# Performance work log

Measured on AMD Instinct MI355X. Metric: run time of the kernel, lower is better.

The kernel has to match this reference:

```python
import jax, jax.numpy as jnp
import numpy as np

N = 4096   # num_nodes == nb_items
E = 3      # num_edge types
C = 2      # num_channels
D = 128    # basket_embed_dim
RU = 128   # rnn_units
B = 32     # batch size
L = 20     # max_seq_length
ALPHA = 0.5


def _gtconv(W, A):
    # softmax over edge types, then channel-weighted combine of adjacencies
    f = jax.nn.softmax(W, axis=1)              # [C, E]
    return jnp.einsum('ce,enm->cnm', f, A)     # [C, N, N]


def _normalize(H):
    # remove self loops, then column-degree (in-degree) inverse normalization
    eye = jnp.eye(H.shape[-1], dtype=H.dtype)
    Hn = H * (1.0 - eye)
    deg = Hn.sum(axis=1)                        # scatter_add over col -> [C, N]
    dinv = jnp.where(deg == 0, jnp.zeros_like(deg), 1.0 / deg)
    dinv = jax.lax.stop_gradient(dinv)          # original computes deg under no_grad
    return Hn * dinv[:, None, :]


def _lstm(x, h0, c0, W_ih, W_hh, b_ih, b_hh):
    # single-layer batch-first LSTM, torch gate order (i, f, g, o)
    def step(carry, xt):
        h, c = carry
        z = xt @ W_ih.T + b_ih + h @ W_hh.T + b_hh
        i, f, g, o = jnp.split(z, 4, axis=-1)
        c = jax.nn.sigmoid(f) * c + jax.nn.sigmoid(i) * jnp.tanh(g)
        h = jax.nn.sigmoid(o) * jnp.tanh(c)
        return (h, c), h
    _, ys = jax.lax.scan(step, (h0, c0), jnp.swapaxes(x, 0, 1))
    return jnp.swapaxes(ys, 0, 1)               # [B, L, RU]


def setup_inputs():
    key = jax.random.key(0)
    k = jax.random.split(key, 12)
    A = jax.random.uniform(k[0], (E, N, N), jnp.float32) * (2.0 / N)
    seqs = (jax.random.uniform(k[1], (B, L, N)) < 0.02).astype(jnp.float32)
    seq_len = jax.random.randint(k[2], (B,), 1, L + 1)
    h0 = jnp.zeros((B, RU), jnp.float32)
    c0 = jnp.zeros((B, RU), jnp.float32)
    W1a = 1.0 + 0.1 * jax.random.normal(k[3], (C, E), jnp.float32)
    W1b = 1.0 + 0.1 * jax.random.normal(k[4], (C, E), jnp.float32)
    W2 = 1.0 + 0.1 * jax.random.normal(k[5], (C, E), jnp.float32)
    I_B = jnp.ones((N,), jnp.float32) / N
    lin_w = jax.random.normal(k[6], (C, D, N), jnp.float32) / np.sqrt(N).astype(np.float32)
    lin_b = jnp.zeros((C, D), jnp.float32)
    proj_w = jax.random.normal(k[7], (D, C * D), jnp.float32) / np.sqrt(C * D).astype(np.float32)
    proj_b = jnp.zeros((D,), jnp.float32)
    W_ih = jax.random.normal(k[8], (4 * RU, D), jnp.float32) / np.sqrt(D).astype(np.float32)
    W_hh = jax.random.normal(k[9], (4 * RU, RU), jnp.float32) / np.sqrt(RU).astype(np.float32)
    b_ih = jnp.zeros((4 * RU,), jnp.float32)
    b_hh = jnp.zeros((4 * RU,), jnp.float32)
    h2item_w = jax.random.normal(k[10], (N, RU), jnp.float32) / np.sqrt(RU).astype(np.float32)
    return dict(A=A, seqs=seqs, seq_len=seq_len, h0=h0, c0=c0, W1a=W1a, W1b=W1b,
                W2=W2, I_B=I_B, lin_w=lin_w, lin_b=lin_b, proj_w=proj_w, proj_b=proj_b,
                W_ih=W_ih, W_hh=W_hh, b_ih=b_ih, b_hh=b_hh, h2item_w=h2item_w)


def reference(A, seqs, seq_len, h0, c0, W1a, W1b, W2, I_B, lin_w, lin_b,
              proj_w, proj_b, W_ih, W_hh, b_ih, b_hh, h2item_w):
    # layer 0 (first=True): H[c] = conv1(A)[c] @ conv2(A)[c]  (spspmm, dense form)
    H = jnp.einsum('cij,cjk->cik', _gtconv(W1a, A), _gtconv(W1b, A))
    # layer 1: H[c] = norm(H)[c] @ conv(A)[c]
    H = jnp.einsum('cij,cjk->cik', _normalize(H), _gtconv(W2, A))

    x = seqs.reshape(-1, N)                     # [B*L, nb_items]
    v = jax.nn.relu(I_B)                        # diag(I_B) after relu
    enc = []
    for i in range(C):
        xh = jax.nn.relu(x @ H[i])
        if i == 0:
            e = jax.nn.relu(x * v) + xh         # note: channel-0 formula differs
        else:
            e = jax.nn.relu(x * v + xh)
        enc.append(e @ lin_w[i].T + lin_b[i])
    enc = jnp.concatenate(enc, axis=1)          # [B*L, C*D]
    baskets = (enc @ proj_w.T + proj_b).reshape(B, L, D)

    lstm_out = _lstm(baskets, h0, c0, W_ih, W_hh, b_ih, b_hh)
    idx = jnp.arange(B) * L + (seq_len - 1)
    last = lstm_out.reshape(-1, RU)[idx]        # [B, RU]
    probs = jax.nn.sigmoid(last @ h2item_w.T)   # [B, nb_items]
    return (1.0 - ALPHA) * probs + ALPHA * (probs * v)
```

## Files before the change

### kernel.cpp

```cpp
#include <hip/hip_runtime.h>


typedef float  f4v  __attribute__((ext_vector_type(4)));
typedef short  s8v  __attribute__((ext_vector_type(8)));
typedef unsigned short u16;
typedef u16    us4  __attribute__((ext_vector_type(4)));

#define NN 4096
#define MM 640

__device__ __forceinline__ u16 f2bf(float f){
  unsigned int u = __float_as_uint(f);
  u += 0x7FFFu + ((u>>16)&1u);
  return (u16)(u>>16);
}
__device__ __forceinline__ float bf2f(u16 h){ return __uint_as_float(((unsigned int)h)<<16); }
__device__ __forceinline__ float sigm(float x){ return 1.f/(1.f+__expf(-x)); }

__device__ __forceinline__ void gload16(const void* g, void* l){
  __builtin_amdgcn_global_load_lds((const __attribute__((address_space(1))) unsigned int*)g,
                                   (__attribute__((address_space(3))) unsigned int*)l, 16, 0, 0);
}

__device__ __forceinline__ void softmax23(const float* __restrict__ W, float f[2][3]){
  #pragma unroll
  for (int c=0;c<2;c++){
    float a=W[c*3+0], b=W[c*3+1], d=W[c*3+2];
    float m=fmaxf(a,fmaxf(b,d));
    float ea=__expf(a-m), eb=__expf(b-m), ed=__expf(d-m);
    float s=1.f/(ea+eb+ed);
    f[c][0]=ea*s; f[c][1]=eb*s; f[c][2]=ed*s;
  }
}

template<int PH3>
__global__ __launch_bounds__(256)
void k_combine(const float* __restrict__ A, const float* __restrict__ Wa,
               const float* __restrict__ Wb, u16* __restrict__ C1,
               u16* __restrict__ Ct, float* __restrict__ r)
{
  __shared__ u16 t2[2][64][68];
  __shared__ float rs[2][64];
  const int tid = threadIdx.x;
  const int n0 = blockIdx.x*64, m0 = blockIdx.y*64;
  float fa[2][3], fb[2][3];
  softmax23(Wa, fa);
  if constexpr(!PH3) softmax23(Wb, fb);
  if constexpr(!PH3){ if (tid < 128) rs[tid>>6][tid&63] = 0.f; }
  __syncthreads();
  const int cl = (tid&15)*4, rw0 = tid>>4;
  float rp[2][4] = {};
  #pragma unroll
  for (int q=0;q<4;q++){
    const int m = q*16 + rw0;
    const float* ap = A + (size_t)(m0+m)*NN + n0 + cl;
    f4v a0 = *(const f4v*)ap;
    f4v a1 = *(const f4v*)(ap + (size_t)NN*NN);
    f4v a2 = *(const f4v*)(ap + 2*(size_t)NN*NN);
    #pragma unroll
    for (int c=0;c<2;c++){
      f4v vt;
      if constexpr(!PH3){
        f4v v1 = fa[c][0]*a0 + fa[c][1]*a1 + fa[c][2]*a2;
        vt     = fb[c][0]*a0 + fb[c][1]*a1 + fb[c][2]*a2;
        us4 o;
        #pragma unroll
        for (int k=0;k<4;k++){ o[k]=f2bf(v1[k]); rp[c][k]+=v1[k]; }
        *(us4*)(C1 + ((size_t)c*NN + m0+m)*NN + n0+cl) = o;
      } else {
        vt = fa[c][0]*a0 + fa[c][1]*a1 + fa[c][2]*a2;
      }
      #pragma unroll
      for (int k=0;k<4;k++) t2[c][cl+k][m] = f2bf(vt[k]);
    }
  }
  if constexpr(!PH3){
    #pragma unroll
    for (int c=0;c<2;c++)
      #pragma unroll
      for (int k=0;k<4;k++) atomicAdd(&rs[c][cl+k], rp[c][k]);
  }
  __syncthreads();
  if constexpr(!PH3){
    if (tid < 128) atomicAdd(&r[(size_t)(tid>>6)*NN + n0 + (tid&63)], rs[tid>>6][tid&63]);
  }
  #pragma unroll
  for (int q=0;q<4;q++){
    const int nl = q*16 + rw0;
    #pragma unroll
    for (int c=0;c<2;c++){
      us4 o = *(const us4*)&t2[c][nl][cl];
      *(us4*)(Ct + ((size_t)c*NN + n0+nl)*NN + m0+cl) = o;
    }
  }
}

__global__ __launch_bounds__(256)
void k_sparse_y(const float* __restrict__ seqs, const u16* __restrict__ C1,
                u16* __restrict__ y)
{
  __shared__ int idxl[512];
  __shared__ int cnt;
  const int tid = threadIdx.x, row = blockIdx.x;
  if (tid==0) cnt = 0;
  __syncthreads();
  const float* xr = seqs + (size_t)row*NN;
  #pragma unroll
  for (int it=0; it<4; ++it){
    f4v v = *(const f4v*)(xr + it*1024 + tid*4);
    #pragma unroll
    for (int k=0;k<4;k++) if (v[k] > 0.5f){ int p = atomicAdd(&cnt,1); if (p<512) idxl[p] = it*1024+tid*4+k; }
  }
  __syncthreads();
  const int nz = cnt < 512 ? cnt : 512;
  float acc0[16], acc1[16];
  #pragma unroll
  for (int k=0;k<16;k++){ acc0[k]=0.f; acc1[k]=0.f; }
  const int cb = tid*16;
  for (int p=0;p<nz;++p){
    const u16* r0 = C1 + (size_t)idxl[p]*NN + cb;
    const u16* r1 = r0 + (size_t)NN*NN;
    s8v a = *(const s8v*)r0, b = *(const s8v*)(r0+8);
    s8v c = *(const s8v*)r1, d = *(const s8v*)(r1+8);
    #pragma unroll
    for (int k=0;k<8;k++){
      acc0[k]   += bf2f((u16)a[k]);
      acc0[8+k] += bf2f((u16)b[k]);
      acc1[k]   += bf2f((u16)c[k]);
      acc1[8+k] += bf2f((u16)d[k]);
    }
  }
  s8v o0,o1,o2,o3;
  #pragma unroll
  for (int k=0;k<8;k++){
    o0[k]=(short)f2bf(acc0[k]);   o1[k]=(short)f2bf(acc0[8+k]);
    o2[k]=(short)f2bf(acc1[k]);   o3[k]=(short)f2bf(acc1[8+k]);
  }
  u16* y0 = y + (size_t)row*NN + cb;
  *(s8v*)y0 = o0; *(s8v*)(y0+8) = o1;
  u16* y1 = y0 + (size_t)MM*NN;
  *(s8v*)y1 = o2; *(s8v*)(y1+8) = o3;
}

__global__ __launch_bounds__(256)
void k_diagdeg(const u16* __restrict__ C1, const u16* __restrict__ C2t,
               const float* __restrict__ r, float* __restrict__ diag1,
               float* __restrict__ dinv)
{
  const int tid = threadIdx.x, lane = tid&63;
  const int gw = blockIdx.x*4 + (tid>>6);
  const int c = gw>>12, k = gw&4095;
  const u16* p1 = C1  + ((size_t)c*NN + k)*NN;
  const u16* p2 = C2t + ((size_t)c*NN + k)*NN;
  const float* pr = r + (size_t)c*NN;
  float dd = 0.f, dg = 0.f;
  for (int it=0; it<8; ++it){
    const int j = it*512 + lane*8;
    s8v v1 = *(const s8v*)(p1+j);
    s8v v2 = *(const s8v*)(p2+j);
    f4v r0 = *(const f4v*)(pr+j);
    f4v r1 = *(const f4v*)(pr+j+4);
    #pragma unroll
    for (int q=0;q<8;q++){
      float c2 = bf2f((u16)v2[q]);
      dd += bf2f((u16)v1[q]) * c2;
      dg += ((q<4)? r0[q] : r1[q-4]) * c2;
    }
  }
  #pragma unroll
  for (int m=1;m<64;m<<=1){ dd += __shfl_xor(dd, m); dg += __shfl_xor(dg, m); }
  if (lane==0){
    float deg = dg - dd;
    diag1[(size_t)c*NN+k] = dd;
    dinv[(size_t)c*NN+k]  = (deg==0.f) ? 0.f : 1.f/deg;
  }
}

template<int EPI>
__global__ __launch_bounds__(256)
void k_gemm(const u16* __restrict__ Xb, const u16* __restrict__ Bt,
            const float* __restrict__ seqs, const float* __restrict__ diag1,
            const float* __restrict__ dinv, const float* __restrict__ IB,
            u16* __restrict__ outp)
{
  __shared__ u16 As[128*32];
  __shared__ u16 Bs[128*32];
  const int tid = threadIdx.x, lane = tid&63, w = tid>>6;
  const int c = blockIdx.z, m0 = blockIdx.x*128, n0 = blockIdx.y*128;
  const u16* Ab = Xb + (size_t)c*MM*NN;
  const u16* Bb = Bt + (size_t)c*NN*NN;
  const int srow = lane>>2, skof = (lane&3)*8;
  const int fr = lane&15, fk = (lane>>4)*8;
  const int wm = (w>>1)*64, wn = (w&1)*64;
  f4v acc[4][4];
  #pragma unroll
  for (int i=0;i<4;i++)
    #pragma unroll
    for (int j=0;j<4;j++) acc[i][j] = (f4v){0.f,0.f,0.f,0.f};
  for (int k0=0;k0<NN;k0+=32){
    gload16(Ab + (size_t)(m0 +      w*16 + srow)*NN + k0 + skof, (void*)&As[(     w*16)*32]);
    gload16(Ab + (size_t)(m0 + 64 + w*16 + srow)*NN + k0 + skof, (void*)&As[(64 + w*16)*32]);
    gload16(Bb + (size_t)(n0 +      w*16 + srow)*NN + k0 + skof, (void*)&Bs[(     w*16)*32]);
    gload16(Bb + (size_t)(n0 + 64 + w*16 + srow)*NN + k0 + skof, (void*)&Bs[(64 + w*16)*32]);
    __syncthreads();
    s8v a[4], b[4];
    #pragma unroll
    for (int t=0;t<4;t++) a[t] = *(const s8v*)&As[(wm + t*16 + fr)*32 + fk];
    #pragma unroll
    for (int t=0;t<4;t++) b[t] = *(const s8v*)&Bs[(wn + t*16 + fr)*32 + fk];
    #pragma unroll
    for (int i=0;i<4;i++)
      #pragma unroll
      for (int j=0;j<4;j++)
        acc[i][j] = __builtin_amdgcn_mfma_f32_16x16x32_bf16(a[i], b[j], acc[i][j], 0, 0, 0);
    __syncthreads();
  }
  #pragma unroll
  for (int i=0;i<4;i++){
    #pragma unroll
    for (int j=0;j<4;j++){
      const int col = n0 + wn + j*16 + fr;
      #pragma unroll
      for (int rr=0;rr<4;rr++){
        const int row = m0 + wm + i*16 + (lane>>4)*4 + rr;
        const float z = acc[i][j][rr];
        const float x = seqs[(size_t)row*NN + col];
        float val;
        if constexpr(EPI==0){
          val = (z - x*diag1[(size_t)c*NN+col]) * dinv[(size_t)c*NN+col];
        } else {
          float xh = fmaxf(z, 0.f);
          float vv = fmaxf(IB[col], 0.f);
          val = (c==0) ? (fmaxf(x*vv,0.f) + xh) : fmaxf(x*vv + xh, 0.f);
        }
        outp[((size_t)c*MM + row)*NN + col] = f2bf(val);
      }
    }
  }
}

__global__ __launch_bounds__(256)
void k_cvt(const float* __restrict__ linw, const float* __restrict__ whh,
           u16* __restrict__ linwb, u16* __restrict__ whhb)
{
  const int g = blockIdx.x*256 + threadIdx.x;
  const int i = g*4;
  const int NL = 2*128*NN;
  f4v v; u16* dst;
  if (i < NL){ v = *(const f4v*)(linw + i); dst = linwb + i; }
  else       { v = *(const f4v*)(whh + (i-NL)); dst = whhb + (i-NL); }
  us4 o;
  #pragma unroll
  for (int k=0;k<4;k++) o[k]=f2bf(v[k]);
  *(us4*)dst = o;
}

__global__ __launch_bounds__(256)
void k_lin(const u16* __restrict__ e, const u16* __restrict__ linwb,
           float* __restrict__ encr)
{
  __shared__ u16 As[64*32];
  __shared__ u16 Bs[64*32];
  const int tid=threadIdx.x, lane=tid&63, w=tid>>6;
  const int m0 = blockIdx.x*64, d0 = blockIdx.y*64;
  const int c = blockIdx.z>>2, ks = blockIdx.z&3;
  const u16* Ab = e + (size_t)c*MM*NN;
  const u16* Bb = linwb + (size_t)c*128*NN;
  const int srow=lane>>2, skof=(lane&3)*8, fr=lane&15, fk=(lane>>4)*8;
  const int wm=(w>>1)*32, wn=(w&1)*32;
  f4v acc[2][2];
  #pragma unroll
  for (int i=0;i<2;i++)
    #pragma unroll
    for (int j=0;j<2;j++) acc[i][j] = (f4v){0.f,0.f,0.f,0.f};
  for (int ki=0;ki<32;++ki){
    const int k0 = ks*1024 + ki*32;
    gload16(Ab + (size_t)(m0 + w*16 + srow)*NN + k0 + skof, (void*)&As[(w*16)*32]);
    gload16(Bb + (size_t)(d0 + w*16 + srow)*NN + k0 + skof, (void*)&Bs[(w*16)*32]);
    __syncthreads();
    s8v a[2], b[2];
    #pragma unroll
    for (int t=0;t<2;t++) a[t] = *(const s8v*)&As[(wm+t*16+fr)*32+fk];
    #pragma unroll
    for (int t=0;t<2;t++) b[t] = *(const s8v*)&Bs[(wn+t*16+fr)*32+fk];
    #pragma unroll
    for (int i=0;i<2;i++)
      #pragma unroll
      for (int j=0;j<2;j++)
        acc[i][j] = __builtin_amdgcn_mfma_f32_16x16x32_bf16(a[i], b[j], acc[i][j], 0, 0, 0);
    __syncthreads();
  }
  #pragma unroll
  for (int i=0;i<2;i++)
    #pragma unroll
    for (int j=0;j<2;j++){
      const int col = d0 + wn + j*16 + fr;
      #pragma unroll
      for (int rr=0;rr<4;rr++){
        const int row = m0 + wm + i*16 + (lane>>4)*4 + rr;
        atomicAdd(&encr[(size_t)row*256 + c*128 + col], acc[i][j][rr]);
      }
    }
}

__global__ __launch_bounds__(256)
void k_proj(const float* __restrict__ encr, const float* __restrict__ linb,
            const float* __restrict__ pw, const float* __restrict__ pb,
            float* __restrict__ bask)
{
  const int g = blockIdx.x*256 + threadIdx.x;
  const int row = g>>7, d = g&127;
  const float* er = encr + (size_t)row*256;
  const float* wr = pw + (size_t)d*256;
  float acc = pb[d];
  for (int j=0;j<256;j+=4){
    f4v e4 = *(const f4v*)(er+j);
    f4v l4 = *(const f4v*)(linb+j);
    f4v w4 = *(const f4v*)(wr+j);
    acc += (e4[0]+l4[0])*w4[0] + (e4[1]+l4[1])*w4[1] + (e4[2]+l4[2])*w4[2] + (e4[3]+l4[3])*w4[3];
  }
  bask[g] = acc;
}

__global__ __launch_bounds__(256)
void k_xhat(const float* __restrict__ bask, const float* __restrict__ wih,
            const float* __restrict__ bih, const float* __restrict__ bhh,
            float* __restrict__ xh)
{
  const int g = blockIdx.x*256 + threadIdx.x;
  const int row = g>>9, n = g&511;
  const float* br = bask + (size_t)row*128;
  const float* wr = wih + (size_t)n*128;
  float acc = bih[n] + bhh[n];
  for (int k=0;k<128;k+=4){
    f4v b4=*(const f4v*)(br+k); f4v w4=*(const f4v*)(wr+k);
    acc += b4[0]*w4[0]+b4[1]*w4[1]+b4[2]*w4[2]+b4[3]*w4[3];
  }
  const int b = row/20, t = row%20;
  xh[((size_t)t*32 + b)*512 + n] = acc;
}

__global__ __launch_bounds__(512)
void k_lstm(const float* __restrict__ xhat, const u16* __restrict__ whhb,
            const float* __restrict__ h0, const float* __restrict__ c0,
            const int* __restrict__ slen, float* __restrict__ last)
{
  __shared__ float zb[32][512];
  __shared__ float cbuf[32][128];
  __shared__ u16 hb[32][136];
  const int tid = threadIdx.x, lane = tid&63, w = tid>>6;
  for (int i=tid; i<4096; i+=512){ int b=i>>7,u=i&127; cbuf[b][u]=c0[i]; hb[b][u]=f2bf(h0[i]); }
  const int fr = lane&15, fko = (lane>>4)*8;
  s8v bfr[4][4];
  #pragma unroll
  for (int nt=0;nt<4;nt++)
    #pragma unroll
    for (int kf=0;kf<4;kf++)
      bfr[nt][kf] = *(const s8v*)(whhb + (size_t)(w*64 + nt*16 + fr)*128 + kf*32 + fko);
  __syncthreads();
  for (int t=0;t<20;++t){
    s8v af[2][4];
    #pragma unroll
    for (int mt=0;mt<2;mt++)
      #pragma unroll
      for (int kf=0;kf<4;kf++)
        af[mt][kf] = *(const s8v*)&hb[mt*16+fr][kf*32+fko];
    f4v z[2][4];
    #pragma unroll
    for (int mt=0;mt<2;mt++)
      #pragma unroll
      for (int nt=0;nt<4;nt++){
        const int nn2 = w*64 + nt*16 + fr;
        #pragma unroll
        for (int rr=0;rr<4;rr++){
          const int bb = mt*16 + (lane>>4)*4 + rr;
          z[mt][nt][rr] = xhat[((size_t)t*32 + bb)*512 + nn2];
        }
      }
    #pragma unroll
    for (int kf=0;kf<4;kf++)
      #pragma unroll
      for (int mt=0;mt<2;mt++)
        #pragma unroll
        for (int nt=0;nt<4;nt++)
          z[mt][nt] = __builtin_amdgcn_mfma_f32_16x16x32_bf16(af[mt][kf], bfr[nt][kf], z[mt][nt], 0, 0, 0);
    #pragma unroll
    for (int mt=0;mt<2;mt++)
      #pragma unroll
      for (int nt=0;nt<4;nt++){
        const int nn2 = w*64 + nt*16 + fr;
        #pragma unroll
        for (int rr=0;rr<4;rr++){
          const int bb = mt*16 + (lane>>4)*4 + rr;
          zb[bb][nn2] = z[mt][nt][rr];
        }
      }
    __syncthreads();
    for (int p=tid; p<4096; p+=512){
      const int b=p>>7, u=p&127;
      float zi=zb[b][u], zf=zb[b][128+u], zg=zb[b][256+u], zo=zb[b][384+u];
      float ii=sigm(zi), ff=sigm(zf), gg=tanhf(zg), oo=sigm(zo);
      float cn = ff*cbuf[b][u] + ii*gg;
      float hn = oo*tanhf(cn);
      cbuf[b][u]=cn; hb[b][u]=f2bf(hn);
      if (t == slen[b]-1) last[p] = hn;
    }
    __syncthreads();
  }
}

__global__ __launch_bounds__(256)
void k_final(const float* __restrict__ last, const float* __restrict__ h2w,
             const float* __restrict__ IB, float* __restrict__ out)
{
  __shared__ float ls[128];
  const int b = blockIdx.y;
  const int n = blockIdx.x*256 + threadIdx.x;
  if (threadIdx.x < 128) ls[threadIdx.x] = last[b*128 + threadIdx.x];
  __syncthreads();
  const float* wr = h2w + (size_t)n*128;
  float acc = 0.f;
  for (int k=0;k<128;k+=4){
    f4v w4 = *(const f4v*)(wr+k);
    acc += w4[0]*ls[k] + w4[1]*ls[k+1] + w4[2]*ls[k+2] + w4[3]*ls[k+3];
  }
  const float vn = fmaxf(IB[n], 0.f);
  out[(size_t)b*NN + n] = (0.5f + 0.5f*vn) * sigm(acc);
}

extern "C" void kernel_launch(void* const* d_in, const int* in_sizes, int n_in,
                              void* d_out, int out_size, void* d_ws, size_t ws_size,
                              hipStream_t stream)
{
  const float* A    = (const float*)d_in[0];
  const float* seqs = (const float*)d_in[1];
  const int*   slen = (const int*)  d_in[2];
  const float* h0   = (const float*)d_in[3];
  const float* c0   = (const float*)d_in[4];
  const float* W1a  = (const float*)d_in[5];
  const float* W1b  = (const float*)d_in[6];
  const float* W2   = (const float*)d_in[7];
  const float* IB   = (const float*)d_in[8];
  const float* linw = (const float*)d_in[9];
  const float* linb = (const float*)d_in[10];
  const float* pw   = (const float*)d_in[11];
  const float* pb   = (const float*)d_in[12];
  const float* wih  = (const float*)d_in[13];
  const float* whh  = (const float*)d_in[14];
  const float* bih  = (const float*)d_in[15];
  const float* bhh  = (const float*)d_in[16];
  const float* h2w  = (const float*)d_in[17];
  (void)in_sizes; (void)n_in; (void)out_size; (void)ws_size;

  char* ws = (char*)d_ws;
  size_t off = 0;
  auto alloc = [&](size_t sz)->void*{ void* p = ws + off; off += (sz + 255) & ~(size_t)255; return p; };
  u16*   C1    = (u16*)  alloc((size_t)2*NN*NN*2);
  u16*   C2t   = (u16*)  alloc((size_t)2*NN*NN*2);
  u16*   y     = (u16*)  alloc((size_t)2*MM*NN*2);
  u16*   u     = (u16*)  alloc((size_t)2*MM*NN*2);
  float* r     = (float*)alloc((size_t)2*NN*4);
  float* diag1 = (float*)alloc((size_t)2*NN*4);
  float* dinv  = (float*)alloc((size_t)2*NN*4);
  u16*   linwb = (u16*)  alloc((size_t)2*128*NN*2);
  u16*   whhb  = (u16*)  alloc((size_t)512*128*2);
  float* encr  = (float*)alloc((size_t)MM*256*4);
  float* bask  = (float*)alloc((size_t)MM*128*4);
  float* xh    = (float*)alloc((size_t)20*32*512*4);
  float* last  = (float*)alloc((size_t)32*128*4);

  hipMemsetAsync(r, 0, (size_t)2*NN*4, stream);
  hipMemsetAsync(encr, 0, (size_t)MM*256*4, stream);

  k_combine<0><<<dim3(64,64),256,0,stream>>>(A, W1a, W1b, C1, C2t, r);
  k_sparse_y<<<MM,256,0,stream>>>(seqs, C1, y);
  k_diagdeg<<<2048,256,0,stream>>>(C1, C2t, r, diag1, dinv);
  k_gemm<0><<<dim3(5,32,2),256,0,stream>>>(y, C2t, seqs, diag1, dinv, IB, u);
  k_combine<1><<<dim3(64,64),256,0,stream>>>(A, W2, W2, C1, C1, r);
  u16* e = y;
  k_gemm<1><<<dim3(5,32,2),256,0,stream>>>(u, C1, seqs, diag1, dinv, IB, e);
  k_cvt<<<1088,256,0,stream>>>(linw, whh, linwb, whhb);
  k_lin<<<dim3(10,2,8),256,0,stream>>>(e, linwb, encr);
  k_proj<<<320,256,0,stream>>>(encr, linb, pw, pb, bask);
  k_xhat<<<1280,256,0,stream>>>(bask, wih, bih, bhh, xh);
  k_lstm<<<1,512,0,stream>>>(xh, whhb, h0, c0, slen, last);
  k_final<<<dim3(16,32),256,0,stream>>>(last, h2w, IB, (float*)d_out);
}
```

Before: 629.8 us.

## Split-K the dense GEMMs, swizzle LDS tiles, and fuse combine passes over A

Both dense 640x4096x4096 GEMMs now split K four ways, so the grid grows from 320 to 1280 blocks. Each block writes fp32 partial sums, and a separate epilogue kernel adds them and applies the normalization or relu logic. The K-tile doubles to 64 and uses an XOR-swizzled LDS layout to cut bank conflicts. The two passes over A that built the combined adjacencies are merged into one kernel that also produces the W2-combined transposed matrix, so A is read once. The cost is about 84 MB of fp32 partial traffic per GEMM, an extra 64 MB workspace matrix, and two more launches.

```diff
diff --git a/kernel.cpp b/kernel.cpp
--- a/kernel.cpp
+++ b/kernel.cpp
@@ -8,6 +8,8 @@
 
 #define NN 4096
 #define MM 640
+#define KSPL 4
+#define KCH (NN/KSPL)
 
 __device__ __forceinline__ u16 f2bf(float f){
   unsigned int u = __float_as_uint(f);
@@ -33,20 +35,22 @@
   }
 }
 
-template<int PH3>
-__global__ __launch_bounds__(256)
-void k_combine(const float* __restrict__ A, const float* __restrict__ Wa,
-               const float* __restrict__ Wb, u16* __restrict__ C1,
-               u16* __restrict__ Ct, float* __restrict__ r)
+__global__ __launch_bounds__(256)
+void k_combine_all(const float* __restrict__ A, const float* __restrict__ W1a,
+                   const float* __restrict__ W1b, const float* __restrict__ W2,
+                   u16* __restrict__ C1, u16* __restrict__ C2t,
+                   u16* __restrict__ C3t, float* __restrict__ r)
 {
   __shared__ u16 t2[2][64][68];
+  __shared__ u16 t3[2][64][68];
   __shared__ float rs[2][64];
   const int tid = threadIdx.x;
   const int n0 = blockIdx.x*64, m0 = blockIdx.y*64;
-  float fa[2][3], fb[2][3];
-  softmax23(Wa, fa);
-  if constexpr(!PH3) softmax23(Wb, fb);
-  if constexpr(!PH3){ if (tid < 128) rs[tid>>6][tid&63] = 0.f; }
+  float fa[2][3], fb[2][3], fc[2][3];
+  softmax23(W1a, fa);
+  softmax23(W1b, fb);
+  softmax23(W2,  fc);
+  if (tid < 128) rs[tid>>6][tid&63] = 0.f;
   __syncthreads();
   const int cl = (tid&15)*4, rw0 = tid>>4;
   float rp[2][4] = {};
@@ -59,38 +63,32 @@
     f4v a2 = *(const f4v*)(ap + 2*(size_t)NN*NN);
     #pragma unroll
     for (int c=0;c<2;c++){
-      f4v vt;
-      if constexpr(!PH3){
-        f4v v1 = fa[c][0]*a0 + fa[c][1]*a1 + fa[c][2]*a2;
-        vt     = fb[c][0]*a0 + fb[c][1]*a1 + fb[c][2]*a2;
-        us4 o;
-        #pragma unroll
-        for (int k=0;k<4;k++){ o[k]=f2bf(v1[k]); rp[c][k]+=v1[k]; }
-        *(us4*)(C1 + ((size_t)c*NN + m0+m)*NN + n0+cl) = o;
-      } else {
-        vt = fa[c][0]*a0 + fa[c][1]*a1 + fa[c][2]*a2;
-      }
-      #pragma unroll
-      for (int k=0;k<4;k++) t2[c][cl+k][m] = f2bf(vt[k]);
-    }
-  }
-  if constexpr(!PH3){
-    #pragma unroll
-    for (int c=0;c<2;c++)
-      #pragma unroll
-      for (int k=0;k<4;k++) atomicAdd(&rs[c][cl+k], rp[c][k]);
-  }
+      f4v v1 = fa[c][0]*a0 + fa[c][1]*a1 + fa[c][2]*a2;
+      f4v vt = fb[c][0]*a0 + fb[c][1]*a1 + fb[c][2]*a2;
+      f4v v3 = fc[c][0]*a0 + fc[c][1]*a1 + fc[c][2]*a2;
+      us4 o;
+      #pragma unroll
+      for (int k=0;k<4;k++){ o[k]=f2bf(v1[k]); rp[c][k]+=v1[k]; }
+      *(us4*)(C1 + ((size_t)c*NN + m0+m)*NN + n0+cl) = o;
+      #pragma unroll
+      for (int k=0;k<4;k++){ t2[c][cl+k][m] = f2bf(vt[k]); t3[c][cl+k][m] = f2bf(v3[k]); }
+    }
+  }
+  #pragma unroll
+  for (int c=0;c<2;c++)
+    #pragma unroll
+    for (int k=0;k<4;k++) atomicAdd(&rs[c][cl+k], rp[c][k]);
   __syncthreads();
-  if constexpr(!PH3){
-    if (tid < 128) atomicAdd(&r[(size_t)(tid>>6)*NN + n0 + (tid&63)], rs[tid>>6][tid&63]);
-  }
+  if (tid < 128) atomicAdd(&r[(size_t)(tid>>6)*NN + n0 + (tid&63)], rs[tid>>6][tid&63]);
   #pragma unroll
   for (int q=0;q<4;q++){
     const int nl = q*16 + rw0;
     #pragma unroll
     for (int c=0;c<2;c++){
-      us4 o = *(const us4*)&t2[c][nl][cl];
-      *(us4*)(Ct + ((size_t)c*NN + n0+nl)*NN + m0+cl) = o;
+      us4 o2 = *(const us4*)&t2[c][nl][cl];
+      us4 o3 = *(const us4*)&t3[c][nl][cl];
+      *(us4*)(C2t + ((size_t)c*NN + n0+nl)*NN + m0+cl) = o2;
+      *(us4*)(C3t + ((size_t)c*NN + n0+nl)*NN + m0+cl) = o3;
     }
   }
 }
@@ -176,45 +174,49 @@
   }
 }
 
-template<int EPI>
-__global__ __launch_bounds__(256)
-void k_gemm(const u16* __restrict__ Xb, const u16* __restrict__ Bt,
-            const float* __restrict__ seqs, const float* __restrict__ diag1,
-            const float* __restrict__ dinv, const float* __restrict__ IB,
-            u16* __restrict__ outp)
-{
-  __shared__ u16 As[128*32];
-  __shared__ u16 Bs[128*32];
+__global__ __launch_bounds__(256)
+void k_gemm_sk(const u16* __restrict__ Xb, const u16* __restrict__ Bt,
+               float* __restrict__ part)
+{
+  __shared__ u16 As[128*64];
+  __shared__ u16 Bs[128*64];
   const int tid = threadIdx.x, lane = tid&63, w = tid>>6;
-  const int c = blockIdx.z, m0 = blockIdx.x*128, n0 = blockIdx.y*128;
+  const int m0 = blockIdx.x*128, n0 = blockIdx.y*128;
+  const int c = blockIdx.z>>2, ks = blockIdx.z&3;
   const u16* Ab = Xb + (size_t)c*MM*NN;
   const u16* Bb = Bt + (size_t)c*NN*NN;
-  const int srow = lane>>2, skof = (lane&3)*8;
-  const int fr = lane&15, fk = (lane>>4)*8;
+  const int srow = lane>>3;
+  const int scol = ((lane&7) ^ srow)*8;
+  const int fr = lane&15, fkq = lane>>4;
   const int wm = (w>>1)*64, wn = (w&1)*64;
-  f4v acc[4][4];
-  #pragma unroll
-  for (int i=0;i<4;i++)
-    #pragma unroll
-    for (int j=0;j<4;j++) acc[i][j] = (f4v){0.f,0.f,0.f,0.f};
-  for (int k0=0;k0<NN;k0+=32){
-    gload16(Ab + (size_t)(m0 +      w*16 + srow)*NN + k0 + skof, (void*)&As[(     w*16)*32]);
-    gload16(Ab + (size_t)(m0 + 64 + w*16 + srow)*NN + k0 + skof, (void*)&As[(64 + w*16)*32]);
-    gload16(Bb + (size_t)(n0 +      w*16 + srow)*NN + k0 + skof, (void*)&Bs[(     w*16)*32]);
-    gload16(Bb + (size_t)(n0 + 64 + w*16 + srow)*NN + k0 + skof, (void*)&Bs[(64 + w*16)*32]);
+  f4v acc[4][4] = {};
+  const int kbase = ks*KCH;
+  for (int k0=0;k0<KCH;k0+=64){
+    #pragma unroll
+    for (int t=0;t<4;t++){
+      gload16(Ab + (size_t)(m0 + t*32 + w*8 + srow)*NN + kbase + k0 + scol, (void*)&As[(t*32 + w*8)*64]);
+      gload16(Bb + (size_t)(n0 + t*32 + w*8 + srow)*NN + kbase + k0 + scol, (void*)&Bs[(t*32 + w*8)*64]);
+    }
     __syncthreads();
-    s8v a[4], b[4];
-    #pragma unroll
-    for (int t=0;t<4;t++) a[t] = *(const s8v*)&As[(wm + t*16 + fr)*32 + fk];
-    #pragma unroll
-    for (int t=0;t<4;t++) b[t] = *(const s8v*)&Bs[(wn + t*16 + fr)*32 + fk];
-    #pragma unroll
-    for (int i=0;i<4;i++)
-      #pragma unroll
-      for (int j=0;j<4;j++)
-        acc[i][j] = __builtin_amdgcn_mfma_f32_16x16x32_bf16(a[i], b[j], acc[i][j], 0, 0, 0);
+    #pragma unroll
+    for (int kk=0;kk<2;kk++){
+      s8v a[4], b[4];
+      #pragma unroll
+      for (int t=0;t<4;t++){
+        const int ra = wm + t*16 + fr;
+        a[t] = *(const s8v*)&As[ra*64 + (((kk*4 + fkq) ^ (ra&7))*8)];
+        const int rb = wn + t*16 + fr;
+        b[t] = *(const s8v*)&Bs[rb*64 + (((kk*4 + fkq) ^ (rb&7))*8)];
+      }
+      #pragma unroll
+      for (int i=0;i<4;i++)
+        #pragma unroll
+        for (int j=0;j<4;j++)
+          acc[i][j] = __builtin_amdgcn_mfma_f32_16x16x32_bf16(a[i], b[j], acc[i][j], 0, 0, 0);
+    }
     __syncthreads();
   }
+  float* pb = part + (size_t)blockIdx.z*MM*NN;
   #pragma unroll
   for (int i=0;i<4;i++){
     #pragma unroll
@@ -223,20 +225,46 @@
       #pragma unroll
       for (int rr=0;rr<4;rr++){
         const int row = m0 + wm + i*16 + (lane>>4)*4 + rr;
-        const float z = acc[i][j][rr];
-        const float x = seqs[(size_t)row*NN + col];
-        float val;
-        if constexpr(EPI==0){
-          val = (z - x*diag1[(size_t)c*NN+col]) * dinv[(size_t)c*NN+col];
-        } else {
-          float xh = fmaxf(z, 0.f);
-          float vv = fmaxf(IB[col], 0.f);
-          val = (c==0) ? (fmaxf(x*vv,0.f) + xh) : fmaxf(x*vv + xh, 0.f);
-        }
-        outp[((size_t)c*MM + row)*NN + col] = f2bf(val);
+        pb[(size_t)row*NN + col] = acc[i][j][rr];
       }
     }
   }
+}
+
+template<int EPI>
+__global__ __launch_bounds__(256)
+void k_epi(const float* __restrict__ part, const float* __restrict__ seqs,
+           const float* __restrict__ diag1, const float* __restrict__ dinv,
+           const float* __restrict__ IB, u16* __restrict__ outp)
+{
+  const int g = blockIdx.x*256 + threadIdx.x;
+  const int c = blockIdx.y;
+  const int row = g>>10, colq = g&1023;
+  const int col = colq*4;
+  const size_t base = (size_t)row*NN + col;
+  f4v z = {0.f,0.f,0.f,0.f};
+  #pragma unroll
+  for (int ks=0;ks<KSPL;ks++)
+    z += *(const f4v*)(part + (size_t)(c*KSPL+ks)*MM*NN + base);
+  f4v x = *(const f4v*)(seqs + base);
+  f4v val;
+  if constexpr(EPI==0){
+    f4v d  = *(const f4v*)(diag1 + (size_t)c*NN + col);
+    f4v dv = *(const f4v*)(dinv  + (size_t)c*NN + col);
+    val = (z - x*d) * dv;
+  } else {
+    f4v ib = *(const f4v*)(IB + col);
+    #pragma unroll
+    for (int k=0;k<4;k++){
+      float xh = fmaxf(z[k], 0.f);
+      float vv = fmaxf(ib[k], 0.f);
+      val[k] = (c==0) ? (fmaxf(x[k]*vv,0.f) + xh) : fmaxf(x[k]*vv + xh, 0.f);
+    }
+  }
+  us4 o;
+  #pragma unroll
+  for (int k=0;k<4;k++) o[k]=f2bf(val[k]);
+  *(us4*)(outp + (size_t)c*MM*NN + base) = o;
 }
 
 __global__ __launch_bounds__(256)
@@ -457,8 +485,10 @@
   auto alloc = [&](size_t sz)->void*{ void* p = ws + off; off += (sz + 255) & ~(size_t)255; return p; };
   u16*   C1    = (u16*)  alloc((size_t)2*NN*NN*2);
   u16*   C2t   = (u16*)  alloc((size_t)2*NN*NN*2);
+  u16*   C3t   = (u16*)  alloc((size_t)2*NN*NN*2);
   u16*   y     = (u16*)  alloc((size_t)2*MM*NN*2);
   u16*   u     = (u16*)  alloc((size_t)2*MM*NN*2);
+  float* part  = (float*)alloc((size_t)2*KSPL*MM*NN*4);
   float* r     = (float*)alloc((size_t)2*NN*4);
   float* diag1 = (float*)alloc((size_t)2*NN*4);
   float* dinv  = (float*)alloc((size_t)2*NN*4);
@@ -472,13 +502,14 @@
   hipMemsetAsync(r, 0, (size_t)2*NN*4, stream);
   hipMemsetAsync(encr, 0, (size_t)MM*256*4, stream);
 
-  k_combine<0><<<dim3(64,64),256,0,stream>>>(A, W1a, W1b, C1, C2t, r);
+  k_combine_all<<<dim3(64,64),256,0,stream>>>(A, W1a, W1b, W2, C1, C2t, C3t, r);
   k_sparse_y<<<MM,256,0,stream>>>(seqs, C1, y);
   k_diagdeg<<<2048,256,0,stream>>>(C1, C2t, r, diag1, dinv);
-  k_gemm<0><<<dim3(5,32,2),256,0,stream>>>(y, C2t, seqs, diag1, dinv, IB, u);
-  k_combine<1><<<dim3(64,64),256,0,stream>>>(A, W2, W2, C1, C1, r);
+  k_gemm_sk<<<dim3(5,32,2*KSPL),256,0,stream>>>(y, C2t, part);
+  k_epi<0><<<dim3(2560,2),256,0,stream>>>(part, seqs, diag1, dinv, IB, u);
+  k_gemm_sk<<<dim3(5,32,2*KSPL),256,0,stream>>>(u, C3t, part);
   u16* e = y;
-  k_gemm<1><<<dim3(5,32,2),256,0,stream>>>(u, C1, seqs, diag1, dinv, IB, e);
+  k_epi<1><<<dim3(2560,2),256,0,stream>>>(part, seqs, diag1, dinv, IB, e);
   k_cvt<<<1088,256,0,stream>>>(linw, whh, linwb, whhb);
   k_lin<<<dim3(10,2,8),256,0,stream>>>(e, linwb, encr);
   k_proj<<<320,256,0,stream>>>(encr, linb, pw, pb, bask);
```

New measurement: 575.9 us. 8.6% less time.
